# Performance work log

Measured on AMD Instinct MI355X. Metric: run time of the kernel, lower is better.

## Reference

```python
import jax, jax.numpy as jnp
import numpy as np

D_MODEL = 64
D_STATE = 16
D_CONV = 4
EXPAND = 2
D_INNER = EXPAND * D_MODEL        # 128
DT_RANK = max(1, D_MODEL // 16)   # 4 (mamba_ssm default ceil(d_model/16))
BATCH, HH, WW = 2, 128, 128


def setup_inputs() -> dict:
    key = jax.random.key(0)
    ks = jax.random.split(key, 10)
    def norm(k, shape, sc=0.05):
        return jax.random.normal(k, shape, jnp.float32) * sc
    # A initialized as in mamba_ssm: A = 1..d_state per channel, stored as log
    A_log = jnp.log(jnp.tile(jnp.arange(1, D_STATE + 1, dtype=jnp.float32), (4, D_INNER, 1)))
    return {
        "x": jax.random.normal(ks[0], (BATCH, D_MODEL, HH, WW), jnp.float32),
        "in_w": norm(ks[1], (4, 2 * D_INNER, D_MODEL)),
        "conv_w": norm(ks[2], (4, D_INNER, D_CONV), 0.2),
        "conv_b": jnp.zeros((4, D_INNER), jnp.float32),
        "xp_w": norm(ks[3], (4, DT_RANK + 2 * D_STATE, D_INNER)),
        "dtp_w": norm(ks[4], (4, D_INNER, DT_RANK), 0.2),
        "dtp_b": jnp.full((4, D_INNER), -4.0, jnp.float32) + norm(ks[5], (4, D_INNER), 0.5),
        "A_log": A_log,
        "Dp": jnp.ones((4, D_INNER), jnp.float32),
        "out_w": norm(ks[6], (4, D_MODEL, D_INNER)),
        "fuse_w": norm(ks[7], (D_MODEL, 4 * D_MODEL)),
        "fuse_b": jnp.zeros((D_MODEL,), jnp.float32),
        "ln_g": jnp.ones((D_MODEL,), jnp.float32),
        "ln_b": jnp.zeros((D_MODEL,), jnp.float32),
    }


def _mamba(xseq, in_w, conv_w, conv_b, xp_w, dtp_w, dtp_b, A_log, Dp, out_w):
    # xseq: (N, L, d_model) -> (N, L, d_model). Single-direction Mamba block.
    N, L, _ = xseq.shape
    xz = xseq @ in_w.T                       # (N, L, 2*d_inner)
    u, z = jnp.split(xz, 2, axis=-1)
    # causal depthwise conv1d, kernel width D_CONV
    up = jnp.pad(u, ((0, 0), (D_CONV - 1, 0), (0, 0)))
    uc = conv_b + sum(up[:, k:k + L, :] * conv_w[:, k][None, None, :] for k in range(D_CONV))
    uc = jax.nn.silu(uc)
    dbl = uc @ xp_w.T                        # (N, L, dt_rank + 2*d_state)
    dt = jax.nn.softplus(dbl[..., :DT_RANK] @ dtp_w.T + dtp_b)   # (N, L, d_inner)
    Bm = dbl[..., DT_RANK:DT_RANK + D_STATE]                     # (N, L, d_state)
    Cm = dbl[..., DT_RANK + D_STATE:]                            # (N, L, d_state)
    A = -jnp.exp(A_log)                                          # (d_inner, d_state)

    def step(h, inp):
        dt_t, B_t, C_t, u_t = inp            # (N,d_inner),(N,d_state),(N,d_state),(N,d_inner)
        h = h * jnp.exp(dt_t[..., None] * A) + (dt_t * u_t)[..., None] * B_t[:, None, :]
        y = jnp.einsum('nds,ns->nd', h, C_t)
        return h, y

    h0 = jnp.zeros((N, D_INNER, D_STATE), xseq.dtype)
    _, ys = jax.lax.scan(step, h0, (dt.swapaxes(0, 1), Bm.swapaxes(0, 1),
                                    Cm.swapaxes(0, 1), uc.swapaxes(0, 1)))
    y = ys.swapaxes(0, 1) + uc * Dp
    y = y * jax.nn.silu(z)
    return y @ out_w.T


def reference(x, in_w, conv_w, conv_b, xp_w, dtp_w, dtp_b, A_log, Dp, out_w,
              fuse_w, fuse_b, ln_g, ln_b):
    B, C, H, W = x.shape
    xhwc = x.transpose(0, 2, 3, 1)           # (B,H,W,C)
    xwhc = x.transpose(0, 3, 2, 1)           # (B,W,H,C)
    d0 = xhwc.reshape(B * H, W, C)                         # horizontal fwd
    d1 = xhwc[:, :, ::-1, :].reshape(B * H, W, C)          # horizontal bwd
    d2 = xwhc.reshape(B * W, H, C)                         # vertical fwd
    d3 = xwhc[:, :, ::-1, :].reshape(B * W, H, C)          # vertical bwd
    xd = jnp.stack([d0, d1, d2, d3])         # (4, B*S, S, C) since H == W
    ys = jax.vmap(_mamba)(xd, in_w, conv_w, conv_b, xp_w, dtp_w, dtp_b, A_log, Dp, out_w)
    y0 = ys[0].reshape(B, H, W, C)
    y1 = ys[1].reshape(B, H, W, C)[:, :, ::-1, :]
    y2 = ys[2].reshape(B, W, H, C).transpose(0, 2, 1, 3)
    y3 = ys[3].reshape(B, W, H, C)[:, :, ::-1, :].transpose(0, 2, 1, 3)
    cat = jnp.concatenate([y0, y1, y2, y3], axis=-1)       # (B,H,W,4C)
    f = cat @ fuse_w.T + fuse_b                            # 1x1 conv
    mu = f.mean(-1, keepdims=True)
    var = f.var(-1, keepdims=True)
    f = (f - mu) * jax.lax.rsqrt(var + 1e-5) * ln_g + ln_b # LayerNorm over C
    f = jax.nn.silu(f)
    return f.transpose(0, 3, 1, 2)                          # (B,C,H,W)
```

## Files before the change

### kernel.cpp

```cpp
#include <hip/hip_runtime.h>
#include <hip/hip_bf16.h>
#include <math.h>


typedef __attribute__((ext_vector_type(8))) short short8;
typedef __attribute__((ext_vector_type(4))) float f32x4;
typedef __attribute__((ext_vector_type(2))) float f32x2;

__device__ __forceinline__ f32x2 pk_mul(f32x2 a, f32x2 b) {
  f32x2 d;
  asm("v_pk_mul_f32 %0, %1, %2" : "=v"(d) : "v"(a), "v"(b));
  return d;
}
__device__ __forceinline__ f32x2 pk_fma(f32x2 a, f32x2 b, f32x2 c) {
  f32x2 d;
  asm("v_pk_fma_f32 %0, %1, %2, %3" : "=v"(d) : "v"(a), "v"(b), "v"(c));
  return d;
}

__device__ __forceinline__ unsigned int pk2bf(float a, float b) {
  __hip_bfloat162 h = __float22bfloat162_rn(make_float2(a, b));
  unsigned int u;
  __builtin_memcpy(&u, &h, 4);
  return u;
}
__device__ __forceinline__ unsigned short f2bf(float f) {
  __hip_bfloat16 h = __float2bfloat16(f);
  unsigned short s;
  __builtin_memcpy(&s, &h, 2);
  return s;
}
__device__ __forceinline__ float bf2f(unsigned short h) {
  return __uint_as_float(((unsigned int)h) << 16);
}
__device__ __forceinline__ float fastrcp(float x) { return __builtin_amdgcn_rcpf(x); }
__device__ __forceinline__ float siluf(float x) { return x * fastrcp(1.f + __expf(-x)); }

__global__ void k0_prep(const float* __restrict__ out_w, const float* __restrict__ fuse_w,
                        const float* __restrict__ in_w, const float* __restrict__ xp_w,
                        const float* __restrict__ x,
                        unsigned short* __restrict__ MT16, unsigned short* __restrict__ W16,
                        unsigned short* __restrict__ XW16, unsigned short* __restrict__ XH,
                        unsigned short* __restrict__ XW) {
  __shared__ unsigned short sT[64*132];
  int blk = blockIdx.x;
  int tid = threadIdx.x;
  if (blk < 128) {
    int idx = blk * 256 + tid;
    int d   = idx & 127;
    int o   = (idx >> 7) & 63;
    int dir = idx >> 13;
    float acc = 0.f;
    #pragma unroll 8
    for (int j = 0; j < 64; ++j)
      acc += out_w[(dir*64 + j)*128 + d] * fuse_w[o*256 + dir*64 + j];
    MT16[o*512 + dir*128 + d] = f2bf(acc);
  } else if (blk < 160) {
    int t = (blk - 128) * 256 + tid;
    int base = t * 8;
    float4 v0 = *(const float4*)(in_w + base);
    float4 v1 = *(const float4*)(in_w + base + 4);
    uint4 pk;
    pk.x = pk2bf(v0.x, v0.y);
    pk.y = pk2bf(v0.z, v0.w);
    pk.z = pk2bf(v1.x, v1.y);
    pk.w = pk2bf(v1.z, v1.w);
    *(uint4*)(W16 + base) = pk;
  } else if (blk < 164) {
    int t = (blk - 160) * 256 + tid;
    for (int pid = t; pid < 4*48*128; pid += 1024) {
      int dir = pid / 6144;
      int rem = pid - dir*6144;
      int row = rem >> 7, c = rem & 127;
      XW16[pid] = (row < 36) ? f2bf(xp_w[dir*4608 + row*128 + c]) : (unsigned short)0;
    }
  } else {
    int idx = blk - 164;
    int b = idx >> 7, h = idx & 127;
    for (int f = tid*4; f < 8192; f += 1024) {
      int c = f >> 7, w = f & 127;
      float4 v = *(const float4*)(x + (((size_t)(b*64 + c)*128 + h)*128 + w));
      sT[c*132 + w + 0] = f2bf(v.x);
      sT[c*132 + w + 1] = f2bf(v.y);
      sT[c*132 + w + 2] = f2bf(v.z);
      sT[c*132 + w + 3] = f2bf(v.w);
    }
    __syncthreads();
    for (int f = tid*8; f < 8192; f += 2048) {
      int w = f >> 6, c0 = f & 63;
      unsigned int pk[4];
      #pragma unroll
      for (int p = 0; p < 4; ++p) {
        unsigned int lo = sT[(c0 + p*2 + 0)*132 + w];
        unsigned int hi = sT[(c0 + p*2 + 1)*132 + w];
        pk[p] = lo | (hi << 16);
      }
      uint4 v; v.x = pk[0]; v.y = pk[1]; v.z = pk[2]; v.w = pk[3];
      *(uint4*)(XH + (((size_t)(b*128 + h)*128 + w)*64 + c0)) = v;
      *(uint4*)(XW + (((size_t)(b*128 + w)*128 + h)*64 + c0)) = v;
    }
  }
}

__global__ __launch_bounds__(256, 3) void k1_front(
    const unsigned short* __restrict__ XH, const unsigned short* __restrict__ XW,
    const unsigned short* __restrict__ W16, const unsigned short* __restrict__ XW16,
    const float* __restrict__ conv_w, const float* __restrict__ conv_b,
    const float* __restrict__ dtp_w, const float* __restrict__ dtp_b,
    const float* __restrict__ A_log, const float* __restrict__ Dp,
    unsigned short* __restrict__ YF)
{
  __shared__ __align__(16) char smem[53248];
  float* sBCf         = (float*)smem;
  unsigned short* sUC = (unsigned short*)(smem + 18432);

  const int tid = threadIdx.x;
  const int dir = blockIdx.x >> 8;
  const int n   = blockIdx.x & 255;
  const int b   = n >> 7;
  const int r   = n & 127;
  const int n_all = dir*256 + n;

  const unsigned short* xsrc = (dir < 2 ? XH : XW) + ((size_t)(b*128 + r)*128)*64;

  const int wave = tid >> 6;
  const int lane = tid & 63;
  const int m16 = lane & 15;
  const int quad = lane >> 4;
  const int tb0 = wave * 32;
  const int st0 = tb0 + m16;
  const int st1 = tb0 + 16 + m16;
  const int sp0 = (dir & 1) ? (127 - st0) : st0;
  const int sp1 = (dir & 1) ? (127 - st1) : st1;

  unsigned int zpk[2][8][2];

  {
    short8 bfr[2][2];
    #pragma unroll
    for (int ks = 0; ks < 2; ++ks) {
      bfr[0][ks] = *(const short8*)(xsrc + sp0*64 + ks*32 + quad*8);
      bfr[1][ks] = *(const short8*)(xsrc + sp1*64 + ks*32 + quad*8);
    }
    const unsigned short* Wd = W16 + (size_t)dir * 16384;

    for (int rt = 0; rt < 8; ++rt) {
      short8 af[2];
      #pragma unroll
      for (int ks = 0; ks < 2; ++ks)
        af[ks] = *(const short8*)(Wd + (rt*16 + m16)*64 + ks*32 + quad*8);
      #pragma unroll
      for (int tt = 0; tt < 2; ++tt) {
        f32x4 acc = {0.f, 0.f, 0.f, 0.f};
        acc = __builtin_amdgcn_mfma_f32_16x16x32_bf16(af[0], bfr[tt][0], acc, 0, 0, 0);
        acc = __builtin_amdgcn_mfma_f32_16x16x32_bf16(af[1], bfr[tt][1], acc, 0, 0, 0);
        const int tok = tt ? st1 : st0;
        const int r0 = rt*16 + quad*4;
        uint2 u2;
        u2.x = pk2bf(acc[0], acc[1]);
        u2.y = pk2bf(acc[2], acc[3]);
        *(uint2*)(sUC + tok*136 + r0) = u2;
      }
    }
    #pragma unroll
    for (int k = 0; k < 8; ++k) {
      short8 af[2];
      #pragma unroll
      for (int ks = 0; ks < 2; ++ks)
        af[ks] = *(const short8*)(Wd + ((8+k)*16 + m16)*64 + ks*32 + quad*8);
      #pragma unroll
      for (int tt = 0; tt < 2; ++tt) {
        f32x4 acc = {0.f, 0.f, 0.f, 0.f};
        acc = __builtin_amdgcn_mfma_f32_16x16x32_bf16(af[0], bfr[tt][0], acc, 0, 0, 0);
        acc = __builtin_amdgcn_mfma_f32_16x16x32_bf16(af[1], bfr[tt][1], acc, 0, 0, 0);
        zpk[tt][k][0] = pk2bf(siluf(acc[0]), siluf(acc[1]));
        zpk[tt][k][1] = pk2bf(siluf(acc[2]), siluf(acc[3]));
      }
    }
  }
  __syncthreads();

  {
    const int d = tid & 127;
    const int half = tid >> 7;
    const int ca = half * 32;
    const int cb2 = (half + 2) * 32;
    const float* cw = conv_w + (size_t)(dir*128 + d)*4;
    const float c0w = cw[0], c1w = cw[1], c2w = cw[2], c3w = cw[3];
    const float cbv = conv_b[dir*128 + d];
    const f32x2 cw0v = {c0w, c0w}, cw1v = {c1w, c1w}, cw2v = {c2w, c2w}, cw3v = {c3w, c3w};
    const f32x2 cbv2 = {cbv, cbv};
    f32x2 A0 = { half ? bf2f(sUC[(ca-3)*136 + d]) : 0.f, bf2f(sUC[(cb2-3)*136 + d]) };
    f32x2 A1 = { half ? bf2f(sUC[(ca-2)*136 + d]) : 0.f, bf2f(sUC[(cb2-2)*136 + d]) };
    f32x2 A2 = { half ? bf2f(sUC[(ca-1)*136 + d]) : 0.f, bf2f(sUC[(cb2-1)*136 + d]) };
    __syncthreads();
    unsigned short* pa = sUC + ca*136 + d;
    unsigned short* pb = sUC + cb2*136 + d;
    for (int i = 0; i < 32; ++i) {
      f32x2 cur = { bf2f(*pa), bf2f(*pb) };
      f32x2 v = pk_fma(cw3v, cur,
                pk_fma(cw2v, A2,
                pk_fma(cw1v, A1,
                pk_fma(cw0v, A0, cbv2))));
      *pa = f2bf(siluf(v.x));
      *pb = f2bf(siluf(v.y));
      A0 = A1; A1 = A2; A2 = cur;
      pa += 136; pb += 136;
    }
  }
  __syncthreads();

  {
    short8 bfr[2][4];
    #pragma unroll
    for (int tt = 0; tt < 2; ++tt)
      #pragma unroll
      for (int ks = 0; ks < 4; ++ks)
        bfr[tt][ks] = *(const short8*)(sUC + (tt ? st1 : st0)*136 + ks*32 + quad*8);

    const unsigned short* XWd = XW16 + (size_t)dir * (48*128);

    for (int rt = 0; rt < 3; ++rt) {
      short8 af[4];
      #pragma unroll
      for (int ks = 0; ks < 4; ++ks)
        af[ks] = *(const short8*)(XWd + (rt*16 + m16)*128 + ks*32 + quad*8);
      #pragma unroll
      for (int tt = 0; tt < 2; ++tt) {
        f32x4 acc = {0.f, 0.f, 0.f, 0.f};
        #pragma unroll
        for (int ks = 0; ks < 4; ++ks)
          acc = __builtin_amdgcn_mfma_f32_16x16x32_bf16(af[ks], bfr[tt][ks], acc, 0, 0, 0);
        const int tok = tt ? st1 : st0;
        const int r0 = rt*16 + quad*4;
        if (r0 == 0) {
          float4 v; v.x = acc[0]; v.y = acc[1]; v.z = acc[2]; v.w = acc[3];
          *(float4*)(smem + 18432 + tok*272 + 256) = v;
        } else if (r0 < 36) {
          float4 v; v.x = acc[0]; v.y = acc[1]; v.z = acc[2]; v.w = acc[3];
          *(float4*)(sBCf + tok*36 + (r0 - 4)) = v;
        }
      }
    }
  }
  __syncthreads();

  {
    const int d = tid >> 1;
    const int p = tid & 1;
    const float* dwp = dtp_w + (size_t)(dir*128 + d) * 4;
    const float dw0 = dwp[0], dw1 = dwp[1], dw2 = dwp[2], dw3 = dwp[3];
    const float db = dtp_b[dir*128 + d];
    const float dpv = Dp[dir*128 + d];

    float Av[8];
    bool fast = true;
    #pragma unroll
    for (int j = 0; j < 8; ++j) {
      float a = -__expf(A_log[((size_t)(dir*128 + d))*16 + p*8 + j]);
      Av[j] = a;
      if (fabsf((-a) - (float)(p*8 + j + 1)) > 1e-3f) fast = false;
    }

    if (fast) {
      f32x2 h0 = {0.f, 0.f}, h1 = {0.f, 0.f}, h2v = {0.f, 0.f}, h3 = {0.f, 0.f};
      const char* qp = smem + 18432 + 256;
      const float* bp = sBCf + p*8;
      const float* cp = sBCf + 16 + p*8;
      const unsigned short* up = sUC + d;
      unsigned short* yo = sUC + d;
      for (int l = 0; l < 128; ++l) {
        float4 Q = *(const float4*)qp;
        f32x2 B01 = *(const f32x2*)(bp + 0), B23 = *(const f32x2*)(bp + 2);
        f32x2 B45 = *(const f32x2*)(bp + 4), B67 = *(const f32x2*)(bp + 6);
        f32x2 C01 = *(const f32x2*)(cp + 0), C23 = *(const f32x2*)(cp + 2);
        f32x2 C45 = *(const f32x2*)(cp + 4), C67 = *(const f32x2*)(cp + 6);
        float u = bf2f(*up);
        float dr = Q.x*dw0 + Q.y*dw1 + Q.z*dw2 + Q.w*dw3 + db;
        float te = __expf(dr);
        float dt = (dr > 20.f) ? dr : __logf(1.f + te);
        float dtu = dt * u;
        float E = fastrcp(1.f + te);
        float E2 = E*E, E4 = E2*E2, E8 = E4*E4;
        float eb = p ? E8 : 1.f;
        f32x2 P0 = {E*eb, E2*eb};
        f32x2 E2v = {E2, E2};
        f32x2 P1 = pk_mul(P0, E2v);
        f32x2 P2 = pk_mul(P1, E2v);
        f32x2 P3 = pk_mul(P2, E2v);
        f32x2 du = {dtu, dtu};
        h0  = pk_fma(h0,  P0, pk_mul(du, B01));
        h1  = pk_fma(h1,  P1, pk_mul(du, B23));
        h2v = pk_fma(h2v, P2, pk_mul(du, B45));
        h3  = pk_fma(h3,  P3, pk_mul(du, B67));
        f32x2 ya = pk_mul(h0, C01);
        f32x2 yb = pk_mul(h1, C23);
        ya = pk_fma(h2v, C45, ya);
        yb = pk_fma(h3,  C67, yb);
        float ypar = (ya.x + ya.y) + (yb.x + yb.y);
        float ot = __uint_as_float((unsigned int)__builtin_amdgcn_mov_dpp(
                     (int)__float_as_uint(ypar), 0xB1, 0xF, 0xF, true));
        float ysum = ypar + ot;
        *yo = f2bf(ysum + u*dpv);
        qp += 272; bp += 36; cp += 36; up += 136; yo += 136;
      }
    } else {
      float h[8];
      #pragma unroll
      for (int j = 0; j < 8; ++j) h[j] = 0.f;
      for (int l = 0; l < 128; ++l) {
        float4 Q = *(const float4*)(smem + 18432 + l*272 + 256);
        float4 b0 = *(const float4*)(sBCf + l*36 + p*8);
        float4 b1 = *(const float4*)(sBCf + l*36 + p*8 + 4);
        float4 c0 = *(const float4*)(sBCf + l*36 + 16 + p*8);
        float4 c1 = *(const float4*)(sBCf + l*36 + 16 + p*8 + 4);
        float Bv[8] = {b0.x,b0.y,b0.z,b0.w, b1.x,b1.y,b1.z,b1.w};
        float Cv[8] = {c0.x,c0.y,c0.z,c0.w, c1.x,c1.y,c1.z,c1.w};
        float u = bf2f(sUC[l*136 + d]);
        float dr = Q.x*dw0 + Q.y*dw1 + Q.z*dw2 + Q.w*dw3 + db;
        float te = __expf(dr);
        float dt = (dr > 20.f) ? dr : __logf(1.f + te);
        float dtu = dt * u;
        float yp = 0.f;
        #pragma unroll
        for (int j = 0; j < 8; ++j) {
          float ej = __expf(dt*Av[j]);
          h[j] = h[j]*ej + dtu*Bv[j];
          yp += h[j]*Cv[j];
        }
        float ot = __uint_as_float((unsigned int)__builtin_amdgcn_mov_dpp(
                     (int)__float_as_uint(yp), 0xB1, 0xF, 0xF, true));
        float ysum = yp + ot;
        if (p == 0) sUC[l*136 + d] = f2bf(ysum + u*dpv);
      }
    }
  }
  __syncthreads();

  #pragma unroll
  for (int tt = 0; tt < 2; ++tt) {
    const int st = tt ? st1 : st0;
    size_t rowbase;
    if (dir < 2)       rowbase = ((size_t)n_all*128 + st)*128;
    else if (dir == 2) rowbase = ((size_t)(512 + b*128 + st)*128 + r)*128;
    else               rowbase = ((size_t)(768 + b*128 + (127-st))*128 + r)*128;
    #pragma unroll
    for (int k = 0; k < 8; ++k) {
      const int dz = 16*k + quad*4;
      uint2 yv = *(const uint2*)(sUC + st*136 + dz);
      float y0 = __uint_as_float(yv.x << 16);
      float y1 = __uint_as_float(yv.x & 0xffff0000u);
      float y2 = __uint_as_float(yv.y << 16);
      float y3 = __uint_as_float(yv.y & 0xffff0000u);
      unsigned int z01 = zpk[tt][k][0], z23 = zpk[tt][k][1];
      float z0 = __uint_as_float(z01 << 16);
      float z1 = __uint_as_float(z01 & 0xffff0000u);
      float z2 = __uint_as_float(z23 << 16);
      float z3 = __uint_as_float(z23 & 0xffff0000u);
      uint2 ov;
      ov.x = pk2bf(y0*z0, y1*z1);
      ov.y = pk2bf(y2*z2, y3*z3);
      *(uint2*)(YF + rowbase + dz) = ov;
    }
  }
}

__global__ __launch_bounds__(512, 2) void k3_fuse(
    const unsigned short* __restrict__ YF, const unsigned short* __restrict__ MT16,
    const float* __restrict__ fuse_b, const float* __restrict__ ln_g,
    const float* __restrict__ ln_b, float* __restrict__ out)
{
  __shared__ __align__(16) unsigned short sYB[64*520];
  __shared__ float sLN[2][64][2];

  const int tid = threadIdx.x;
  const int blk = blockIdx.x;
  const int b = blk >> 8;
  const int rr2 = blk & 255;
  const int h = rr2 >> 1;
  const int w0 = (rr2 & 1) * 64;

  for (int f = tid*8; f < 32768; f += 4096) {
    int dirg = f >> 13;
    int rem = f & 8191;
    int tok = rem >> 7;
    int dd = rem & 127;
    int X = (dirg == 1) ? (127 - w0 - tok) : (w0 + tok);
    size_t base = ((size_t)(dirg*256 + b*128 + h)*128 + X)*128 + dd;
    *(uint4*)(sYB + tok*520 + dirg*128 + dd) = *(const uint4*)(YF + base);
  }
  __syncthreads();

  const int wave = tid >> 6;
  const int lane = tid & 63;
  const int m16 = lane & 15;
  const int quad = lane >> 4;
  const int tg   = wave & 3;
  const int mh   = wave >> 2;
  const int tok  = tg*16 + m16;

  short8 bfr[16];
  #pragma unroll
  for (int jt = 0; jt < 16; ++jt)
    bfr[jt] = *(const short8*)(sYB + tok*520 + jt*32 + quad*8);

  float facc[2][4];
  #pragma unroll
  for (int mi = 0; mi < 2; ++mi) {
    const int mt = mh*2 + mi;
    f32x4 acc = {0.f, 0.f, 0.f, 0.f};
    #pragma unroll
    for (int jt = 0; jt < 16; ++jt) {
      short8 af = *(const short8*)(MT16 + (size_t)(mt*16 + m16)*512 + jt*32 + quad*8);
      acc = __builtin_amdgcn_mfma_f32_16x16x32_bf16(af, bfr[jt], acc, 0, 0, 0);
    }
    facc[mi][0] = acc[0]; facc[mi][1] = acc[1]; facc[mi][2] = acc[2]; facc[mi][3] = acc[3];
  }

  float fv[8];
  float s1 = 0.f, s2 = 0.f;
  #pragma unroll
  for (int mi = 0; mi < 2; ++mi)
    #pragma unroll
    for (int rr = 0; rr < 4; ++rr) {
      int o = (mh*2 + mi)*16 + quad*4 + rr;
      float v = facc[mi][rr] + fuse_b[o];
      fv[mi*4 + rr] = v;
      s1 += v; s2 += v*v;
    }
  s1 += __shfl_xor(s1, 16, 64); s1 += __shfl_xor(s1, 32, 64);
  s2 += __shfl_xor(s2, 16, 64); s2 += __shfl_xor(s2, 32, 64);
  if (lane < 16) {
    sLN[mh][tok][0] = s1;
    sLN[mh][tok][1] = s2;
  }
  __syncthreads();
  float t1 = s1 + sLN[1 - mh][tok][0];
  float t2 = s2 + sLN[1 - mh][tok][1];
  float mu = t1 * (1.f/64.f);
  float var = t2 * (1.f/64.f) - mu*mu;
  float rs = rsqrtf(var + 1e-5f);

  #pragma unroll
  for (int mi = 0; mi < 2; ++mi)
    #pragma unroll
    for (int rr = 0; rr < 4; ++rr) {
      int o = (mh*2 + mi)*16 + quad*4 + rr;
      float v = (fv[mi*4 + rr] - mu) * rs * ln_g[o] + ln_b[o];
      out[((size_t)(b*64 + o)*128 + h)*128 + (w0 + tok)] = siluf(v);
    }
}

extern "C" void kernel_launch(void* const* d_in, const int* in_sizes, int n_in,
                              void* d_out, int out_size, void* d_ws, size_t ws_size,
                              hipStream_t stream) {
  const float* x      = (const float*)d_in[0];
  const float* in_w   = (const float*)d_in[1];
  const float* conv_w = (const float*)d_in[2];
  const float* conv_b = (const float*)d_in[3];
  const float* xp_w   = (const float*)d_in[4];
  const float* dtp_w  = (const float*)d_in[5];
  const float* dtp_b  = (const float*)d_in[6];
  const float* A_log  = (const float*)d_in[7];
  const float* Dp     = (const float*)d_in[8];
  const float* out_w  = (const float*)d_in[9];
  const float* fuse_w = (const float*)d_in[10];
  const float* fuse_b = (const float*)d_in[11];
  const float* ln_g   = (const float*)d_in[12];
  const float* ln_b   = (const float*)d_in[13];
  float* out = (float*)d_out;

  char* ws = (char*)d_ws;
  unsigned short* YF   = (unsigned short*)(ws);
  unsigned short* MT16 = (unsigned short*)(ws + 33554432);
  unsigned short* W16  = (unsigned short*)(ws + 33619968);
  unsigned short* XW16 = (unsigned short*)(ws + 33751040);
  unsigned short* XH   = (unsigned short*)(ws + 33800192);
  unsigned short* XWt  = (unsigned short*)(ws + 37994496);

  k0_prep<<<dim3(420), dim3(256), 0, stream>>>(out_w, fuse_w, in_w, xp_w, x,
                                               MT16, W16, XW16, XH, XWt);
  k1_front<<<dim3(1024), dim3(256), 0, stream>>>(XH, XWt, W16, XW16, conv_w, conv_b,
                                                 dtp_w, dtp_b, A_log, Dp, YF);
  k3_fuse<<<dim3(512), dim3(512), 0, stream>>>(YF, MT16, fuse_b, ln_g, ln_b, out);
}
```

Before: 203.5 us.

## Split SSM scan into two parallel halves with decay-based carry correction

The sequential 128-step selective scan is split into two independent 64-step chains, one per half of the sequence, run interleaved in the same thread to expose instruction-level parallelism. A second 64-step pass then adds the first half's final state, decayed by the cumulative product of per-step decay factors, contracted with C, to the second half's outputs. This shortens the dependent chain but adds a correction pass and an extra bf16 round-trip on the second-half outputs, which may change numerics slightly.

```diff
diff --git a/kernel.cpp b/kernel.cpp
--- a/kernel.cpp
+++ b/kernel.cpp
@@ -35,6 +35,10 @@
 }
 __device__ __forceinline__ float fastrcp(float x) { return __builtin_amdgcn_rcpf(x); }
 __device__ __forceinline__ float siluf(float x) { return x * fastrcp(1.f + __expf(-x)); }
+__device__ __forceinline__ float dpp_swap1(float x) {
+  return __uint_as_float((unsigned int)__builtin_amdgcn_mov_dpp(
+           (int)__float_as_uint(x), 0xB1, 0xF, 0xF, true));
+}
 
 __global__ void k0_prep(const float* __restrict__ out_w, const float* __restrict__ fuse_w,
                         const float* __restrict__ in_w, const float* __restrict__ xp_w,
@@ -263,46 +267,105 @@
     }
 
     if (fast) {
-      f32x2 h0 = {0.f, 0.f}, h1 = {0.f, 0.f}, h2v = {0.f, 0.f}, h3 = {0.f, 0.f};
-      const char* qp = smem + 18432 + 256;
-      const float* bp = sBCf + p*8;
-      const float* cp = sBCf + 16 + p*8;
-      const unsigned short* up = sUC + d;
-      unsigned short* yo = sUC + d;
-      for (int l = 0; l < 128; ++l) {
+      f32x2 ha0 = {0.f,0.f}, ha1 = {0.f,0.f}, ha2 = {0.f,0.f}, ha3 = {0.f,0.f};
+      f32x2 hb0 = {0.f,0.f}, hb1 = {0.f,0.f}, hb2 = {0.f,0.f}, hb3 = {0.f,0.f};
+      const char* qpA = smem + 18432 + 256;
+      const char* qpB = qpA + 64*272;
+      const float* bpA = sBCf + p*8;
+      const float* bpB = sBCf + 64*36 + p*8;
+      const float* cpA = sBCf + 16 + p*8;
+      const float* cpB = sBCf + 64*36 + 16 + p*8;
+      const unsigned short* upA = sUC + d;
+      const unsigned short* upB = sUC + 64*136 + d;
+      unsigned short* yoA = sUC + d;
+      unsigned short* yoB = sUC + 64*136 + d;
+      for (int i = 0; i < 64; ++i) {
+        float4 QA = *(const float4*)qpA;
+        float4 QB = *(const float4*)qpB;
+        float uA = bf2f(*upA);
+        float uB = bf2f(*upB);
+        f32x2 BA01 = *(const f32x2*)(bpA+0), BA23 = *(const f32x2*)(bpA+2);
+        f32x2 BA45 = *(const f32x2*)(bpA+4), BA67 = *(const f32x2*)(bpA+6);
+        f32x2 BB01 = *(const f32x2*)(bpB+0), BB23 = *(const f32x2*)(bpB+2);
+        f32x2 BB45 = *(const f32x2*)(bpB+4), BB67 = *(const f32x2*)(bpB+6);
+        f32x2 CA01 = *(const f32x2*)(cpA+0), CA23 = *(const f32x2*)(cpA+2);
+        f32x2 CA45 = *(const f32x2*)(cpA+4), CA67 = *(const f32x2*)(cpA+6);
+        f32x2 CB01 = *(const f32x2*)(cpB+0), CB23 = *(const f32x2*)(cpB+2);
+        f32x2 CB45 = *(const f32x2*)(cpB+4), CB67 = *(const f32x2*)(cpB+6);
+        float drA = QA.x*dw0 + QA.y*dw1 + QA.z*dw2 + QA.w*dw3 + db;
+        float drB = QB.x*dw0 + QB.y*dw1 + QB.z*dw2 + QB.w*dw3 + db;
+        float teA = __expf(drA), teB = __expf(drB);
+        float dtA = (drA > 20.f) ? drA : __logf(1.f + teA);
+        float dtB = (drB > 20.f) ? drB : __logf(1.f + teB);
+        float duA = dtA * uA, duB = dtB * uB;
+        float EA = fastrcp(1.f + teA), EB = fastrcp(1.f + teB);
+        float EA2 = EA*EA, EA4 = EA2*EA2, EA8 = EA4*EA4;
+        float EB2 = EB*EB, EB4 = EB2*EB2, EB8 = EB4*EB4;
+        float ebA = p ? EA8 : 1.f;
+        float ebB = p ? EB8 : 1.f;
+        f32x2 PA0 = {EA*ebA, EA2*ebA};
+        f32x2 EA2v = {EA2, EA2};
+        f32x2 PA1 = pk_mul(PA0, EA2v);
+        f32x2 PA2 = pk_mul(PA1, EA2v);
+        f32x2 PA3 = pk_mul(PA2, EA2v);
+        f32x2 PB0 = {EB*ebB, EB2*ebB};
+        f32x2 EB2v = {EB2, EB2};
+        f32x2 PB1 = pk_mul(PB0, EB2v);
+        f32x2 PB2 = pk_mul(PB1, EB2v);
+        f32x2 PB3 = pk_mul(PB2, EB2v);
+        f32x2 duAv = {duA, duA}, duBv = {duB, duB};
+        ha0 = pk_fma(ha0, PA0, pk_mul(duAv, BA01));
+        ha1 = pk_fma(ha1, PA1, pk_mul(duAv, BA23));
+        ha2 = pk_fma(ha2, PA2, pk_mul(duAv, BA45));
+        ha3 = pk_fma(ha3, PA3, pk_mul(duAv, BA67));
+        hb0 = pk_fma(hb0, PB0, pk_mul(duBv, BB01));
+        hb1 = pk_fma(hb1, PB1, pk_mul(duBv, BB23));
+        hb2 = pk_fma(hb2, PB2, pk_mul(duBv, BB45));
+        hb3 = pk_fma(hb3, PB3, pk_mul(duBv, BB67));
+        f32x2 ya = pk_mul(ha0, CA01);
+        f32x2 yb = pk_mul(ha1, CA23);
+        ya = pk_fma(ha2, CA45, ya);
+        yb = pk_fma(ha3, CA67, yb);
+        float yA = (ya.x + ya.y) + (yb.x + yb.y);
+        f32x2 za = pk_mul(hb0, CB01);
+        f32x2 zb = pk_mul(hb1, CB23);
+        za = pk_fma(hb2, CB45, za);
+        zb = pk_fma(hb3, CB67, zb);
+        float yB = (za.x + za.y) + (zb.x + zb.y);
+        float sA = yA + dpp_swap1(yA);
+        float sB = yB + dpp_swap1(yB);
+        *yoA = f2bf(sA + uA*dpv);
+        *yoB = f2bf(sB + uB*dpv);
+        qpA += 272; qpB += 272; bpA += 36; bpB += 36; cpA += 36; cpB += 36;
+        upA += 136; upB += 136; yoA += 136; yoB += 136;
+      }
+      float G = 1.f;
+      const char* qp = smem + 18432 + 256 + 64*272;
+      const float* cp = sBCf + 64*36 + 16 + p*8;
+      unsigned short* yo = sUC + 64*136 + d;
+      for (int i = 0; i < 64; ++i) {
         float4 Q = *(const float4*)qp;
-        f32x2 B01 = *(const f32x2*)(bp + 0), B23 = *(const f32x2*)(bp + 2);
-        f32x2 B45 = *(const f32x2*)(bp + 4), B67 = *(const f32x2*)(bp + 6);
-        f32x2 C01 = *(const f32x2*)(cp + 0), C23 = *(const f32x2*)(cp + 2);
-        f32x2 C45 = *(const f32x2*)(cp + 4), C67 = *(const f32x2*)(cp + 6);
-        float u = bf2f(*up);
         float dr = Q.x*dw0 + Q.y*dw1 + Q.z*dw2 + Q.w*dw3 + db;
         float te = __expf(dr);
-        float dt = (dr > 20.f) ? dr : __logf(1.f + te);
-        float dtu = dt * u;
         float E = fastrcp(1.f + te);
-        float E2 = E*E, E4 = E2*E2, E8 = E4*E4;
-        float eb = p ? E8 : 1.f;
-        f32x2 P0 = {E*eb, E2*eb};
-        f32x2 E2v = {E2, E2};
-        f32x2 P1 = pk_mul(P0, E2v);
-        f32x2 P2 = pk_mul(P1, E2v);
-        f32x2 P3 = pk_mul(P2, E2v);
-        f32x2 du = {dtu, dtu};
-        h0  = pk_fma(h0,  P0, pk_mul(du, B01));
-        h1  = pk_fma(h1,  P1, pk_mul(du, B23));
-        h2v = pk_fma(h2v, P2, pk_mul(du, B45));
-        h3  = pk_fma(h3,  P3, pk_mul(du, B67));
-        f32x2 ya = pk_mul(h0, C01);
-        f32x2 yb = pk_mul(h1, C23);
-        ya = pk_fma(h2v, C45, ya);
-        yb = pk_fma(h3,  C67, yb);
-        float ypar = (ya.x + ya.y) + (yb.x + yb.y);
-        float ot = __uint_as_float((unsigned int)__builtin_amdgcn_mov_dpp(
-                     (int)__float_as_uint(ypar), 0xB1, 0xF, 0xF, true));
-        float ysum = ypar + ot;
-        *yo = f2bf(ysum + u*dpv);
-        qp += 272; bp += 36; cp += 36; up += 136; yo += 136;
+        G *= E;
+        float G2 = G*G, G4 = G2*G2, G8 = G4*G4;
+        float eb = p ? G8 : 1.f;
+        f32x2 P0 = {G*eb, G2*eb};
+        f32x2 G2v = {G2, G2};
+        f32x2 P1 = pk_mul(P0, G2v);
+        f32x2 P2 = pk_mul(P1, G2v);
+        f32x2 P3 = pk_mul(P2, G2v);
+        f32x2 C01 = *(const f32x2*)(cp+0), C23 = *(const f32x2*)(cp+2);
+        f32x2 C45 = *(const f32x2*)(cp+4), C67 = *(const f32x2*)(cp+6);
+        f32x2 a = pk_mul(pk_mul(P0, ha0), C01);
+        a = pk_fma(pk_mul(P1, ha1), C23, a);
+        a = pk_fma(pk_mul(P2, ha2), C45, a);
+        a = pk_fma(pk_mul(P3, ha3), C67, a);
+        float corr = a.x + a.y;
+        corr += dpp_swap1(corr);
+        *yo = f2bf(bf2f(*yo) + corr);
+        qp += 272; cp += 36; yo += 136;
       }
     } else {
       float h[8];
@@ -328,8 +391,7 @@
           h[j] = h[j]*ej + dtu*Bv[j];
           yp += h[j]*Cv[j];
         }
-        float ot = __uint_as_float((unsigned int)__builtin_amdgcn_mov_dpp(
-                     (int)__float_as_uint(yp), 0xB1, 0xF, 0xF, true));
+        float ot = dpp_swap1(yp);
         float ysum = yp + ot;
         if (p == 0) sUC[l*136 + d] = f2bf(ysum + u*dpv);
       }
```

New measurement: 229.0 us. 12.5% more time.
